# Kernel optimization log

Measured on AMD Instinct MI355X. Metric: run time of the kernel, lower is better.

Reference implementation:

```python
import jax, jax.numpy as jnp
import numpy as np

B, T, S, H = 8, 512, 512, 128


def setup_inputs() -> dict:
    key = jax.random.key(0)
    ks = jax.random.split(key, 8)
    query = jax.random.normal(ks[0], (B, T, H), dtype=jnp.float32)
    encoder_outputs = jax.random.normal(ks[1], (B, S, H), dtype=jnp.float32)
    src_lengths = jax.random.randint(ks[2], (B,), 1, S + 1)
    src_lengths = src_lengths.at[0].set(S)  # torch mask width == lengths.max() must equal S
    scale = 1.0 / np.sqrt(H)
    W_h = jax.random.normal(ks[3], (H, H), dtype=jnp.float32) * scale
    W_s = jax.random.normal(ks[4], (H, H), dtype=jnp.float32) * scale
    v = jax.random.normal(ks[5], (H,), dtype=jnp.float32) * scale
    W_out_w = jax.random.normal(ks[6], (H, 2 * H), dtype=jnp.float32) * (1.0 / np.sqrt(2 * H))
    W_out_b = jax.random.normal(ks[7], (H,), dtype=jnp.float32) * 0.01
    return {"query": query, "encoder_outputs": encoder_outputs,
            "src_lengths": src_lengths, "W_h": W_h, "W_s": W_s, "v": v,
            "W_out_w": W_out_w, "W_out_b": W_out_b}


def reference(query, encoder_outputs, src_lengths, W_h, W_s, v, W_out_w, W_out_b):
    # query: (B,T,H); encoder_outputs: (B,S,H)
    S_ = encoder_outputs.shape[1]
    WS = jnp.einsum('bth,oh->bto', query, W_s)            # (B,T,H)
    WH = jnp.einsum('bsh,oh->bso', encoder_outputs, W_h)  # (B,S,H)
    # additive scores: v^T tanh(W_s s_t + W_h h_i)  -> (B,T,S)
    scores = jnp.einsum('btsh,h->bts', jnp.tanh(WS[:, :, None, :] + WH[:, None, :, :]), v)
    mask = jnp.arange(S_) < src_lengths[:, None]          # (B,S)
    # faithful quirk: original zeroes (not -inf) masked scores before softmax
    scores = jnp.where(mask[:, None, :], scores, 0.0)
    attn = jax.nn.softmax(scores, axis=-1)                # (B,T,S)
    ct = jnp.einsum('bts,bsh->bth', attn, encoder_outputs)
    concat = jnp.concatenate([ct, query], axis=-1)        # (B,T,2H)
    return jnp.tanh(jnp.einsum('btc,oc->bto', concat, W_out_w) + W_out_b)
```

## Files before the change

### kernel.cpp

```cpp
#include <hip/hip_runtime.h>

#define NB 8
#define NT 512
#define NS 512
#define NH 128
#define C2LOG2E 2.8853900817779268f

__device__ __forceinline__ float fast_exp2(float x) { return __builtin_amdgcn_exp2f(x); }
__device__ __forceinline__ float fast_rcp(float x)  { return __builtin_amdgcn_rcpf(x); }
__device__ __forceinline__ float fast_tanh(float x) {
  float e = fast_exp2(x * C2LOG2E);
  return 1.0f - 2.0f * fast_rcp(e + 1.0f);
}

__device__ __forceinline__ float dot4(float4 a, float4 b) {
  return (a.x * b.x + a.y * b.y) + (a.z * b.z + a.w * b.w);
}

__device__ __forceinline__ float2 pair_acc2(float e0, float e1, float v0, float v1,
                                            float2 f0, float2 f1, float2 acc) {
  float2 P0, P1, num, den;
  P0.x = fmaf(e0, f0.x, 1.0f); P0.y = fmaf(e0, f0.y, 1.0f);
  P1.x = fmaf(e1, f1.x, 1.0f); P1.y = fmaf(e1, f1.y, 1.0f);
  num.x = fmaf(v0, P1.x, v1 * P0.x); num.y = fmaf(v0, P1.y, v1 * P0.y);
  den.x = P0.x * P1.x; den.y = P0.y * P1.y;
  acc.x = fmaf(num.x, fast_rcp(den.x), acc.x);
  acc.y = fmaf(num.y, fast_rcp(den.y), acc.y);
  return acc;
}

__global__ __launch_bounds__(256) void bah_proj_kernel(
    const float* __restrict__ query, const float* __restrict__ enc,
    const float* __restrict__ W_s, const float* __restrict__ W_h,
    const float* __restrict__ Wout, const float* __restrict__ Woutb,
    float* __restrict__ EWS, float* __restrict__ EWHT,
    float* __restrict__ ENCW, float* __restrict__ QW2) {
  __shared__ __align__(16) float lds_w[64 * 132];
  __shared__ __align__(16) float lds_x[32 * 132];
  const int set = blockIdx.x >> 8;
  const int blk = blockIdx.x & 255;
  const int rb = blk >> 1, ch = blk & 1;
  const int r0 = rb * 32, c0 = ch * 64;
  const int tid = threadIdx.x;
  const float* in = (set == 1 || set == 2) ? enc : query;
  const float* Wb; int wst;
  if (set == 0)      { Wb = W_s;        wst = 128; }
  else if (set == 1) { Wb = W_h;        wst = 128; }
  else if (set == 2) { Wb = Wout;       wst = 256; }
  else               { Wb = Wout + 128; wst = 256; }
  for (int i = tid; i < 2048; i += 256) {
    int r = i >> 5, c4 = i & 31;
    *(float4*)(lds_w + r * 132 + c4 * 4) =
        *(const float4*)(Wb + (c0 + r) * wst + c4 * 4);
  }
  for (int i = tid; i < 1024; i += 256) {
    int r = i >> 5, c4 = i & 31;
    *(float4*)(lds_x + r * 132 + c4 * 4) =
        *(const float4*)(in + (r0 + r) * NH + c4 * 4);
  }
  __syncthreads();
  const int cg = tid & 31;
  const int rg = tid >> 5;
  float acc[4][2] = {{0,0},{0,0},{0,0},{0,0}};
  for (int k4 = 0; k4 < 32; ++k4) {
    float4 xa[4], wb[2];
    #pragma unroll
    for (int i = 0; i < 4; ++i)
      xa[i] = *(const float4*)(lds_x + (rg * 4 + i) * 132 + k4 * 4);
    #pragma unroll
    for (int m = 0; m < 2; ++m)
      wb[m] = *(const float4*)(lds_w + (cg + 32 * m) * 132 + k4 * 4);
    #pragma unroll
    for (int i = 0; i < 4; ++i)
      #pragma unroll
      for (int m = 0; m < 2; ++m)
        acc[i][m] += dot4(xa[i], wb[m]);
  }
  if (set == 0) {
    #pragma unroll
    for (int i = 0; i < 4; ++i)
      #pragma unroll
      for (int m = 0; m < 2; ++m)
        EWS[(r0 + rg * 4 + i) * NH + c0 + cg + 32 * m] =
            fast_exp2(C2LOG2E * acc[i][m]);
  } else if (set == 1) {
    __syncthreads();
    #pragma unroll
    for (int i = 0; i < 4; ++i)
      #pragma unroll
      for (int m = 0; m < 2; ++m)
        lds_x[(cg + 32 * m) * 33 + rg * 4 + i] = fast_exp2(C2LOG2E * acc[i][m]);
    __syncthreads();
    const int b = r0 >> 9, sl0 = r0 & 511;
    const int s_lane = tid & 31, hr = tid >> 5;
    #pragma unroll
    for (int j = 0; j < 8; ++j)
      EWHT[b * NH * NS + (c0 + hr * 8 + j) * NS + sl0 + s_lane] =
          lds_x[(hr * 8 + j) * 33 + s_lane];
  } else if (set == 2) {
    #pragma unroll
    for (int i = 0; i < 4; ++i)
      #pragma unroll
      for (int m = 0; m < 2; ++m)
        ENCW[(r0 + rg * 4 + i) * NH + c0 + cg + 32 * m] = acc[i][m];
  } else {
    #pragma unroll
    for (int i = 0; i < 4; ++i)
      #pragma unroll
      for (int m = 0; m < 2; ++m) {
        int c = c0 + cg + 32 * m;
        QW2[(r0 + rg * 4 + i) * NH + c] = acc[i][m] + Woutb[c];
      }
  }
}

__global__ __launch_bounds__(512) void bah_mega_kernel(
    const float* __restrict__ EWS, const float* __restrict__ EWHT,
    const float* __restrict__ v, const float* __restrict__ ENCW,
    const float* __restrict__ QW2, const int* __restrict__ src_len,
    float* __restrict__ out) {
  __shared__ __align__(16) float smem[13824];
  float* s_v   = smem;
  float* s_et  = smem + 128;
  float* s_aT  = smem + 1184;
  float* s_par = smem + 5280;
  float* s_sc  = smem + 9632;
  float* s_red = smem + 13760;

  const int tid = threadIdx.x;
  const int bb = blockIdx.x >> 6;
  const int t0 = (blockIdx.x & 63) * 8;
  const int len = src_len[bb];

  if (tid < 32) *(float4*)(s_v + tid * 4) = *(const float4*)(v + tid * 4);
  if (tid < 256) {
    int r = tid >> 5, c4 = tid & 31;
    *(float4*)(s_et + r * 132 + c4 * 4) =
        *(const float4*)(EWS + (bb * NT + t0 + r) * NH + c4 * 4);
  }
  __syncthreads();

  float V0;
  {
    float2 vv = *(const float2*)(s_v + (tid & 63) * 2);
    V0 = vv.x + vv.y;
    #pragma unroll
    for (int msk = 1; msk <= 32; msk <<= 1)
      V0 += __shfl_xor(V0, msk, 64);
  }

  const int tg = tid >> 8, sp = tid & 255;
  const int sbase = sp * 2;
  const int h0 = tg * 64;
  float2 acc2[8];
  #pragma unroll
  for (int i = 0; i < 8; ++i) { acc2[i].x = 0.f; acc2[i].y = 0.f; }
  const int wave_s0 = (sp & ~63) * 2;
  if (wave_s0 < len) {
    const float* fb = EWHT + bb * NH * NS + h0 * NS + sbase;
    for (int ho = 0; ho < 8; ++ho) {
      const float* fh = fb + ho * 8 * NS;
      float2 F0 = *(const float2*)(fh + 0 * NS);
      float2 F1 = *(const float2*)(fh + 1 * NS);
      float2 F2 = *(const float2*)(fh + 2 * NS);
      float2 F3 = *(const float2*)(fh + 3 * NS);
      float2 F4 = *(const float2*)(fh + 4 * NS);
      float2 F5 = *(const float2*)(fh + 5 * NS);
      float2 F6 = *(const float2*)(fh + 6 * NS);
      float2 F7 = *(const float2*)(fh + 7 * NS);
      float4 va = *(const float4*)(s_v + h0 + ho * 8);
      float4 vb = *(const float4*)(s_v + h0 + ho * 8 + 4);
      #pragma unroll
      for (int tt = 0; tt < 8; ++tt) {
        float4 e0 = *(const float4*)(s_et + tt * 132 + h0 + ho * 8);
        float4 e1 = *(const float4*)(s_et + tt * 132 + h0 + ho * 8 + 4);
        acc2[tt] = pair_acc2(e0.x, e0.y, va.x, va.y, F0, F1, acc2[tt]);
        acc2[tt] = pair_acc2(e0.z, e0.w, va.z, va.w, F2, F3, acc2[tt]);
        acc2[tt] = pair_acc2(e1.x, e1.y, vb.x, vb.y, F4, F5, acc2[tt]);
        acc2[tt] = pair_acc2(e1.z, e1.w, vb.z, vb.w, F6, F7, acc2[tt]);
      }
    }
  }
  if (tg == 1) {
    #pragma unroll
    for (int tt = 0; tt < 8; ++tt)
      *(float2*)(s_par + sp * 17 + tt * 2) = acc2[tt];
  }
  __syncthreads();
  if (tg == 0) {
    #pragma unroll
    for (int tt = 0; tt < 8; ++tt) {
      float2 oth = *(const float2*)(s_par + sp * 17 + tt * 2);
      float sx = acc2[tt].x + oth.x;
      float sy = acc2[tt].y + oth.y;
      float2 r;
      r.x = (sbase + 0 < len) ? fmaf(-2.f, sx, V0) : 0.f;
      r.y = (sbase + 1 < len) ? fmaf(-2.f, sy, V0) : 0.f;
      *(float2*)(s_sc + tt * 516 + sbase) = r;
    }
  }
  __syncthreads();

  const int t = tid & 7;
  const int c = tid >> 3;
  const int wv = tid >> 6;
  float pv[8];
  float mx = -3.4e38f;
  #pragma unroll
  for (int k = 0; k < 8; ++k) {
    pv[k] = s_sc[t * 516 + c + 64 * k];
    mx = fmaxf(mx, pv[k]);
  }
  #pragma unroll
  for (int msk = 8; msk <= 32; msk <<= 1)
    mx = fmaxf(mx, __shfl_xor(mx, msk, 64));
  if ((tid & 63) < 8) s_red[wv * 8 + t] = mx;
  __syncthreads();
  #pragma unroll
  for (int j = 1; j < 8; ++j) mx = fmaxf(mx, s_red[j * 8 + t]);
  mx = fmaxf(mx, s_red[t]);
  __syncthreads();
  float sum = 0.f;
  #pragma unroll
  for (int k = 0; k < 8; ++k) {
    pv[k] = fast_exp2((pv[k] - mx) * 1.4426950408889634f);
    sum += pv[k];
  }
  #pragma unroll
  for (int msk = 8; msk <= 32; msk <<= 1)
    sum += __shfl_xor(sum, msk, 64);
  if ((tid & 63) < 8) s_red[wv * 8 + t] = sum;
  __syncthreads();
  sum = 0.f;
  #pragma unroll
  for (int j = 0; j < 8; ++j) sum += s_red[j * 8 + t];
  const float rd = fast_rcp(sum);
  #pragma unroll
  for (int k = 0; k < 8; ++k)
    s_aT[(c + 64 * k) * 8 + t] = pv[k] * rd;
  __syncthreads();

  const int hg = tid & 31, sg = tid >> 5;
  float4 a8[8] = {{0,0,0,0},{0,0,0,0},{0,0,0,0},{0,0,0,0},
                  {0,0,0,0},{0,0,0,0},{0,0,0,0},{0,0,0,0}};
  const float* eb = ENCW + bb * NS * NH + hg * 4;
  for (int k = 0; k < 32; ++k) {
    int s = sg * 32 + k;
    float4 e  = *(const float4*)(eb + s * NH);
    float4 w0 = *(const float4*)(s_aT + s * 8);
    float4 w1 = *(const float4*)(s_aT + s * 8 + 4);
    a8[0].x += w0.x*e.x; a8[0].y += w0.x*e.y; a8[0].z += w0.x*e.z; a8[0].w += w0.x*e.w;
    a8[1].x += w0.y*e.x; a8[1].y += w0.y*e.y; a8[1].z += w0.y*e.z; a8[1].w += w0.y*e.w;
    a8[2].x += w0.z*e.x; a8[2].y += w0.z*e.y; a8[2].z += w0.z*e.z; a8[2].w += w0.z*e.w;
    a8[3].x += w0.w*e.x; a8[3].y += w0.w*e.y; a8[3].z += w0.w*e.z; a8[3].w += w0.w*e.w;
    a8[4].x += w1.x*e.x; a8[4].y += w1.x*e.y; a8[4].z += w1.x*e.z; a8[4].w += w1.x*e.w;
    a8[5].x += w1.y*e.x; a8[5].y += w1.y*e.y; a8[5].z += w1.y*e.z; a8[5].w += w1.y*e.w;
    a8[6].x += w1.z*e.x; a8[6].y += w1.z*e.y; a8[6].z += w1.z*e.z; a8[6].w += w1.z*e.w;
    a8[7].x += w1.w*e.x; a8[7].y += w1.w*e.y; a8[7].z += w1.w*e.z; a8[7].w += w1.w*e.w;
  }
  #pragma unroll
  for (int i = 0; i < 8; ++i) {
    a8[i].x += __shfl_xor(a8[i].x, 32, 64);
    a8[i].y += __shfl_xor(a8[i].y, 32, 64);
    a8[i].z += __shfl_xor(a8[i].z, 32, 64);
    a8[i].w += __shfl_xor(a8[i].w, 32, 64);
  }
  float* lred = s_par;
  if ((tid & 63) < 32) {
    #pragma unroll
    for (int i = 0; i < 8; ++i)
      *(float4*)(lred + wv * 1024 + i * 128 + hg * 4) = a8[i];
  }
  __syncthreads();
  if (tid < 256) {
    int tt = tid >> 5, hh = tid & 31;
    float4 o = {0.f, 0.f, 0.f, 0.f};
    #pragma unroll
    for (int j = 0; j < 8; ++j) {
      float4 p = *(const float4*)(lred + j * 1024 + tt * 128 + hh * 4);
      o.x += p.x; o.y += p.y; o.z += p.z; o.w += p.w;
    }
    const int row = bb * NT + t0 + tt;
    float4 q4 = *(const float4*)(QW2 + row * NH + hh * 4);
    float4 r;
    r.x = fast_tanh(o.x + q4.x);
    r.y = fast_tanh(o.y + q4.y);
    r.z = fast_tanh(o.z + q4.z);
    r.w = fast_tanh(o.w + q4.w);
    *(float4*)(out + row * NH + hh * 4) = r;
  }
}

extern "C" void kernel_launch(void* const* d_in, const int* in_sizes, int n_in,
                              void* d_out, int out_size, void* d_ws, size_t ws_size,
                              hipStream_t stream) {
  const float* query = (const float*)d_in[0];
  const float* enc   = (const float*)d_in[1];
  const int*   slen  = (const int*)d_in[2];
  const float* W_h   = (const float*)d_in[3];
  const float* W_s   = (const float*)d_in[4];
  const float* v     = (const float*)d_in[5];
  const float* Woutw = (const float*)d_in[6];
  const float* Woutb = (const float*)d_in[7];
  float* out = (float*)d_out;

  float* ws = (float*)d_ws;
  float* EWS  = ws;
  float* EWHT = ws + 524288;
  float* ENCW = ws + 1048576;
  float* QW2  = ws + 1572864;

  bah_proj_kernel<<<1024, 256, 0, stream>>>(query, enc, W_s, W_h, Woutw,
                                            Woutb, EWS, EWHT, ENCW, QW2);
  bah_mega_kernel<<<512, 512, 0, stream>>>(EWS, EWHT, v, ENCW, QW2, slen, out);
}
```

Baseline: 118.1 us.

## Retile attention kernel to 4 queries per block with 4 keys per thread

The fused attention kernel now handles 4 query rows per block with 256 threads instead of 8 rows with 512, and each thread covers 4 source positions using float4 loads of the transposed encoder projection. Shared memory shrinks through buffer aliasing, and launch bounds ask for 4 blocks per CU so more blocks can be resident. The grid doubles to 1024 blocks. In exchange, each EWHT element loaded is reused across only 4 query rows instead of 8, so global and L2 traffic for the score stage roughly doubles.

```diff
diff --git a/kernel.cpp b/kernel.cpp
--- a/kernel.cpp
+++ b/kernel.cpp
@@ -17,15 +17,21 @@
   return (a.x * b.x + a.y * b.y) + (a.z * b.z + a.w * b.w);
 }
 
-__device__ __forceinline__ float2 pair_acc2(float e0, float e1, float v0, float v1,
-                                            float2 f0, float2 f1, float2 acc) {
-  float2 P0, P1, num, den;
+__device__ __forceinline__ float4 pair_acc(float e0, float e1, float v0, float v1,
+                                           float4 f0, float4 f1, float4 acc) {
+  float4 P0, P1, num, den;
   P0.x = fmaf(e0, f0.x, 1.0f); P0.y = fmaf(e0, f0.y, 1.0f);
+  P0.z = fmaf(e0, f0.z, 1.0f); P0.w = fmaf(e0, f0.w, 1.0f);
   P1.x = fmaf(e1, f1.x, 1.0f); P1.y = fmaf(e1, f1.y, 1.0f);
+  P1.z = fmaf(e1, f1.z, 1.0f); P1.w = fmaf(e1, f1.w, 1.0f);
   num.x = fmaf(v0, P1.x, v1 * P0.x); num.y = fmaf(v0, P1.y, v1 * P0.y);
+  num.z = fmaf(v0, P1.z, v1 * P0.z); num.w = fmaf(v0, P1.w, v1 * P0.w);
   den.x = P0.x * P1.x; den.y = P0.y * P1.y;
+  den.z = P0.z * P1.z; den.w = P0.w * P1.w;
   acc.x = fmaf(num.x, fast_rcp(den.x), acc.x);
   acc.y = fmaf(num.y, fast_rcp(den.y), acc.y);
+  acc.z = fmaf(num.z, fast_rcp(den.z), acc.z);
+  acc.w = fmaf(num.w, fast_rcp(den.w), acc.w);
   return acc;
 }
 
@@ -114,26 +120,27 @@
   }
 }
 
-__global__ __launch_bounds__(512) void bah_mega_kernel(
+__global__ __launch_bounds__(256, 4) void bah_mega_kernel(
     const float* __restrict__ EWS, const float* __restrict__ EWHT,
     const float* __restrict__ v, const float* __restrict__ ENCW,
     const float* __restrict__ QW2, const int* __restrict__ src_len,
     float* __restrict__ out) {
-  __shared__ __align__(16) float smem[13824];
-  float* s_v   = smem;
-  float* s_et  = smem + 128;
-  float* s_aT  = smem + 1184;
-  float* s_par = smem + 5280;
-  float* s_sc  = smem + 9632;
-  float* s_red = smem + 13760;
+  __shared__ __align__(16) float smem[4928];
+  float* s_aT  = smem;
+  float* s_par = smem;
+  float* s_sc  = smem + 2176;
+  float* lred  = smem + 2176;
+  float* s_et  = smem + 4240;
+  float* s_v   = smem + 4768;
+  float* s_red = smem + 4896;
 
   const int tid = threadIdx.x;
-  const int bb = blockIdx.x >> 6;
-  const int t0 = (blockIdx.x & 63) * 8;
+  const int bb = blockIdx.x >> 7;
+  const int t0 = (blockIdx.x & 127) * 4;
   const int len = src_len[bb];
 
   if (tid < 32) *(float4*)(s_v + tid * 4) = *(const float4*)(v + tid * 4);
-  if (tid < 256) {
+  if (tid < 128) {
     int r = tid >> 5, c4 = tid & 31;
     *(float4*)(s_et + r * 132 + c4 * 4) =
         *(const float4*)(EWS + (bb * NT + t0 + r) * NH + c4 * 4);
@@ -149,60 +156,58 @@
       V0 += __shfl_xor(V0, msk, 64);
   }
 
-  const int tg = tid >> 8, sp = tid & 255;
-  const int sbase = sp * 2;
+  const int tg = tid >> 7, sp = tid & 127;
+  const int sbase = sp * 4;
   const int h0 = tg * 64;
-  float2 acc2[8];
-  #pragma unroll
-  for (int i = 0; i < 8; ++i) { acc2[i].x = 0.f; acc2[i].y = 0.f; }
-  const int wave_s0 = (sp & ~63) * 2;
+  float4 acc4[4] = {{0,0,0,0},{0,0,0,0},{0,0,0,0},{0,0,0,0}};
+  const int wave_s0 = (sp & 64) * 4;
   if (wave_s0 < len) {
     const float* fb = EWHT + bb * NH * NS + h0 * NS + sbase;
     for (int ho = 0; ho < 8; ++ho) {
       const float* fh = fb + ho * 8 * NS;
-      float2 F0 = *(const float2*)(fh + 0 * NS);
-      float2 F1 = *(const float2*)(fh + 1 * NS);
-      float2 F2 = *(const float2*)(fh + 2 * NS);
-      float2 F3 = *(const float2*)(fh + 3 * NS);
-      float2 F4 = *(const float2*)(fh + 4 * NS);
-      float2 F5 = *(const float2*)(fh + 5 * NS);
-      float2 F6 = *(const float2*)(fh + 6 * NS);
-      float2 F7 = *(const float2*)(fh + 7 * NS);
+      float4 F0 = *(const float4*)(fh + 0 * NS);
+      float4 F1 = *(const float4*)(fh + 1 * NS);
+      float4 F2 = *(const float4*)(fh + 2 * NS);
+      float4 F3 = *(const float4*)(fh + 3 * NS);
+      float4 F4 = *(const float4*)(fh + 4 * NS);
+      float4 F5 = *(const float4*)(fh + 5 * NS);
+      float4 F6 = *(const float4*)(fh + 6 * NS);
+      float4 F7 = *(const float4*)(fh + 7 * NS);
       float4 va = *(const float4*)(s_v + h0 + ho * 8);
       float4 vb = *(const float4*)(s_v + h0 + ho * 8 + 4);
       #pragma unroll
-      for (int tt = 0; tt < 8; ++tt) {
+      for (int tt = 0; tt < 4; ++tt) {
         float4 e0 = *(const float4*)(s_et + tt * 132 + h0 + ho * 8);
         float4 e1 = *(const float4*)(s_et + tt * 132 + h0 + ho * 8 + 4);
-        acc2[tt] = pair_acc2(e0.x, e0.y, va.x, va.y, F0, F1, acc2[tt]);
-        acc2[tt] = pair_acc2(e0.z, e0.w, va.z, va.w, F2, F3, acc2[tt]);
-        acc2[tt] = pair_acc2(e1.x, e1.y, vb.x, vb.y, F4, F5, acc2[tt]);
-        acc2[tt] = pair_acc2(e1.z, e1.w, vb.z, vb.w, F6, F7, acc2[tt]);
+        acc4[tt] = pair_acc(e0.x, e0.y, va.x, va.y, F0, F1, acc4[tt]);
+        acc4[tt] = pair_acc(e0.z, e0.w, va.z, va.w, F2, F3, acc4[tt]);
+        acc4[tt] = pair_acc(e1.x, e1.y, vb.x, vb.y, F4, F5, acc4[tt]);
+        acc4[tt] = pair_acc(e1.z, e1.w, vb.z, vb.w, F6, F7, acc4[tt]);
       }
     }
   }
   if (tg == 1) {
     #pragma unroll
-    for (int tt = 0; tt < 8; ++tt)
-      *(float2*)(s_par + sp * 17 + tt * 2) = acc2[tt];
+    for (int tt = 0; tt < 4; ++tt)
+      *(float4*)(s_par + sp * 17 + tt * 4) = acc4[tt];
   }
   __syncthreads();
   if (tg == 0) {
     #pragma unroll
-    for (int tt = 0; tt < 8; ++tt) {
-      float2 oth = *(const float2*)(s_par + sp * 17 + tt * 2);
-      float sx = acc2[tt].x + oth.x;
-      float sy = acc2[tt].y + oth.y;
-      float2 r;
-      r.x = (sbase + 0 < len) ? fmaf(-2.f, sx, V0) : 0.f;
-      r.y = (sbase + 1 < len) ? fmaf(-2.f, sy, V0) : 0.f;
-      *(float2*)(s_sc + tt * 516 + sbase) = r;
+    for (int tt = 0; tt < 4; ++tt) {
+      float4 oth = *(const float4*)(s_par + sp * 17 + tt * 4);
+      float4 r;
+      r.x = (sbase + 0 < len) ? fmaf(-2.f, acc4[tt].x + oth.x, V0) : 0.f;
+      r.y = (sbase + 1 < len) ? fmaf(-2.f, acc4[tt].y + oth.y, V0) : 0.f;
+      r.z = (sbase + 2 < len) ? fmaf(-2.f, acc4[tt].z + oth.z, V0) : 0.f;
+      r.w = (sbase + 3 < len) ? fmaf(-2.f, acc4[tt].w + oth.w, V0) : 0.f;
+      *(float4*)(s_sc + tt * 516 + sbase) = r;
     }
   }
   __syncthreads();
 
-  const int t = tid & 7;
-  const int c = tid >> 3;
+  const int t = tid & 3;
+  const int c = tid >> 2;
   const int wv = tid >> 6;
   float pv[8];
   float mx = -3.4e38f;
@@ -212,13 +217,12 @@
     mx = fmaxf(mx, pv[k]);
   }
   #pragma unroll
-  for (int msk = 8; msk <= 32; msk <<= 1)
+  for (int msk = 4; msk <= 32; msk <<= 1)
     mx = fmaxf(mx, __shfl_xor(mx, msk, 64));
-  if ((tid & 63) < 8) s_red[wv * 8 + t] = mx;
-  __syncthreads();
-  #pragma unroll
-  for (int j = 1; j < 8; ++j) mx = fmaxf(mx, s_red[j * 8 + t]);
-  mx = fmaxf(mx, s_red[t]);
+  if ((tid & 63) < 4) s_red[wv * 4 + t] = mx;
+  __syncthreads();
+  mx = fmaxf(fmaxf(s_red[t], s_red[4 + t]),
+             fmaxf(s_red[8 + t], s_red[12 + t]));
   __syncthreads();
   float sum = 0.f;
   #pragma unroll
@@ -227,66 +231,55 @@
     sum += pv[k];
   }
   #pragma unroll
-  for (int msk = 8; msk <= 32; msk <<= 1)
+  for (int msk = 4; msk <= 32; msk <<= 1)
     sum += __shfl_xor(sum, msk, 64);
-  if ((tid & 63) < 8) s_red[wv * 8 + t] = sum;
-  __syncthreads();
-  sum = 0.f;
-  #pragma unroll
-  for (int j = 0; j < 8; ++j) sum += s_red[j * 8 + t];
+  if ((tid & 63) < 4) s_red[wv * 4 + t] = sum;
+  __syncthreads();
+  sum = (s_red[t] + s_red[4 + t]) + (s_red[8 + t] + s_red[12 + t]);
   const float rd = fast_rcp(sum);
   #pragma unroll
   for (int k = 0; k < 8; ++k)
-    s_aT[(c + 64 * k) * 8 + t] = pv[k] * rd;
+    s_aT[(c + 64 * k) * 4 + t] = pv[k] * rd;
   __syncthreads();
 
   const int hg = tid & 31, sg = tid >> 5;
-  float4 a8[8] = {{0,0,0,0},{0,0,0,0},{0,0,0,0},{0,0,0,0},
-                  {0,0,0,0},{0,0,0,0},{0,0,0,0},{0,0,0,0}};
+  float4 a4[4] = {{0,0,0,0},{0,0,0,0},{0,0,0,0},{0,0,0,0}};
   const float* eb = ENCW + bb * NS * NH + hg * 4;
-  for (int k = 0; k < 32; ++k) {
-    int s = sg * 32 + k;
-    float4 e  = *(const float4*)(eb + s * NH);
-    float4 w0 = *(const float4*)(s_aT + s * 8);
-    float4 w1 = *(const float4*)(s_aT + s * 8 + 4);
-    a8[0].x += w0.x*e.x; a8[0].y += w0.x*e.y; a8[0].z += w0.x*e.z; a8[0].w += w0.x*e.w;
-    a8[1].x += w0.y*e.x; a8[1].y += w0.y*e.y; a8[1].z += w0.y*e.z; a8[1].w += w0.y*e.w;
-    a8[2].x += w0.z*e.x; a8[2].y += w0.z*e.y; a8[2].z += w0.z*e.z; a8[2].w += w0.z*e.w;
-    a8[3].x += w0.w*e.x; a8[3].y += w0.w*e.y; a8[3].z += w0.w*e.z; a8[3].w += w0.w*e.w;
-    a8[4].x += w1.x*e.x; a8[4].y += w1.x*e.y; a8[4].z += w1.x*e.z; a8[4].w += w1.x*e.w;
-    a8[5].x += w1.y*e.x; a8[5].y += w1.y*e.y; a8[5].z += w1.y*e.z; a8[5].w += w1.y*e.w;
-    a8[6].x += w1.z*e.x; a8[6].y += w1.z*e.y; a8[6].z += w1.z*e.z; a8[6].w += w1.z*e.w;
-    a8[7].x += w1.w*e.x; a8[7].y += w1.w*e.y; a8[7].z += w1.w*e.z; a8[7].w += w1.w*e.w;
-  }
-  #pragma unroll
-  for (int i = 0; i < 8; ++i) {
-    a8[i].x += __shfl_xor(a8[i].x, 32, 64);
-    a8[i].y += __shfl_xor(a8[i].y, 32, 64);
-    a8[i].z += __shfl_xor(a8[i].z, 32, 64);
-    a8[i].w += __shfl_xor(a8[i].w, 32, 64);
-  }
-  float* lred = s_par;
+  for (int k = 0; k < 64; ++k) {
+    int s = sg * 64 + k;
+    float4 e = *(const float4*)(eb + s * NH);
+    float4 w = *(const float4*)(s_aT + s * 4);
+    a4[0].x += w.x*e.x; a4[0].y += w.x*e.y; a4[0].z += w.x*e.z; a4[0].w += w.x*e.w;
+    a4[1].x += w.y*e.x; a4[1].y += w.y*e.y; a4[1].z += w.y*e.z; a4[1].w += w.y*e.w;
+    a4[2].x += w.z*e.x; a4[2].y += w.z*e.y; a4[2].z += w.z*e.z; a4[2].w += w.z*e.w;
+    a4[3].x += w.w*e.x; a4[3].y += w.w*e.y; a4[3].z += w.w*e.z; a4[3].w += w.w*e.w;
+  }
+  #pragma unroll
+  for (int i = 0; i < 4; ++i) {
+    a4[i].x += __shfl_xor(a4[i].x, 32, 64);
+    a4[i].y += __shfl_xor(a4[i].y, 32, 64);
+    a4[i].z += __shfl_xor(a4[i].z, 32, 64);
+    a4[i].w += __shfl_xor(a4[i].w, 32, 64);
+  }
   if ((tid & 63) < 32) {
     #pragma unroll
-    for (int i = 0; i < 8; ++i)
-      *(float4*)(lred + wv * 1024 + i * 128 + hg * 4) = a8[i];
-  }
-  __syncthreads();
-  if (tid < 256) {
+    for (int i = 0; i < 4; ++i)
+      *(float4*)(lred + wv * 512 + i * 128 + hg * 4) = a4[i];
+  }
+  __syncthreads();
+  if (tid < 128) {
     int tt = tid >> 5, hh = tid & 31;
-    float4 o = {0.f, 0.f, 0.f, 0.f};
-    #pragma unroll
-    for (int j = 0; j < 8; ++j) {
-      float4 p = *(const float4*)(lred + j * 1024 + tt * 128 + hh * 4);
-      o.x += p.x; o.y += p.y; o.z += p.z; o.w += p.w;
-    }
+    float4 s0 = *(const float4*)(lred + 0 * 512 + tt * 128 + hh * 4);
+    float4 s1 = *(const float4*)(lred + 1 * 512 + tt * 128 + hh * 4);
+    float4 s2 = *(const float4*)(lred + 2 * 512 + tt * 128 + hh * 4);
+    float4 s3 = *(const float4*)(lred + 3 * 512 + tt * 128 + hh * 4);
     const int row = bb * NT + t0 + tt;
     float4 q4 = *(const float4*)(QW2 + row * NH + hh * 4);
     float4 r;
-    r.x = fast_tanh(o.x + q4.x);
-    r.y = fast_tanh(o.y + q4.y);
-    r.z = fast_tanh(o.z + q4.z);
-    r.w = fast_tanh(o.w + q4.w);
+    r.x = fast_tanh(((s0.x + s1.x) + (s2.x + s3.x)) + q4.x);
+    r.y = fast_tanh(((s0.y + s1.y) + (s2.y + s3.y)) + q4.y);
+    r.z = fast_tanh(((s0.z + s1.z) + (s2.z + s3.z)) + q4.z);
+    r.w = fast_tanh(((s0.w + s1.w) + (s2.w + s3.w)) + q4.w);
     *(float4*)(out + row * NH + hh * 4) = r;
   }
 }
@@ -312,5 +305,5 @@
 
   bah_proj_kernel<<<1024, 256, 0, stream>>>(query, enc, W_s, W_h, Woutw,
                                             Woutb, EWS, EWHT, ENCW, QW2);
-  bah_mega_kernel<<<512, 512, 0, stream>>>(EWS, EWHT, v, ENCW, QW2, slen, out);
-}
+  bah_mega_kernel<<<1024, 256, 0, stream>>>(EWS, EWHT, v, ENCW, QW2, slen, out);
+}
```

Result: slower. 129.8 us (+10.0%).

## Shrink shared memory via aliasing and tree reduction, interleave batch across blocks

Applied to the files above, without the earlier changes.

Cuts the kernel's shared-memory footprint by aliasing buffers whose lifetimes do not overlap and by replacing the 8-way partial-sum buffer with a three-step tree reduction. It also sets a min-blocks hint in launch_bounds and maps consecutive blocks to different batches. The goal is more resident blocks per CU and better load balance across the variable-length batches. In exchange, the final reduction adds several extra barriers and ends with only one wave computing the output.

```diff
diff --git a/kernel.cpp b/kernel.cpp
--- a/kernel.cpp
+++ b/kernel.cpp
@@ -114,22 +114,23 @@
   }
 }
 
-__global__ __launch_bounds__(512) void bah_mega_kernel(
+__global__ __launch_bounds__(512, 8) void bah_mega_kernel(
     const float* __restrict__ EWS, const float* __restrict__ EWHT,
     const float* __restrict__ v, const float* __restrict__ ENCW,
     const float* __restrict__ QW2, const int* __restrict__ src_len,
     float* __restrict__ out) {
-  __shared__ __align__(16) float smem[13824];
-  float* s_v   = smem;
-  float* s_et  = smem + 128;
-  float* s_aT  = smem + 1184;
-  float* s_par = smem + 5280;
-  float* s_sc  = smem + 9632;
-  float* s_red = smem + 13760;
+  __shared__ __align__(16) float smem[9472];
+  float* s_par = smem;
+  float* s_aT  = smem;
+  float* s_sc  = smem + 4096;
+  float* red4  = smem + 4096;
+  float* s_et  = smem + 8224;
+  float* s_v   = smem + 9280;
+  float* s_red = smem + 9408;
 
   const int tid = threadIdx.x;
-  const int bb = blockIdx.x >> 6;
-  const int t0 = (blockIdx.x & 63) * 8;
+  const int bb = blockIdx.x & 7;
+  const int t0 = (blockIdx.x >> 3) * 8;
   const int len = src_len[bb];
 
   if (tid < 32) *(float4*)(s_v + tid * 4) = *(const float4*)(v + tid * 4);
@@ -184,13 +185,13 @@
   if (tg == 1) {
     #pragma unroll
     for (int tt = 0; tt < 8; ++tt)
-      *(float2*)(s_par + sp * 17 + tt * 2) = acc2[tt];
+      *(float2*)(s_par + tt * 512 + sp * 2) = acc2[tt];
   }
   __syncthreads();
   if (tg == 0) {
     #pragma unroll
     for (int tt = 0; tt < 8; ++tt) {
-      float2 oth = *(const float2*)(s_par + sp * 17 + tt * 2);
+      float2 oth = *(const float2*)(s_par + tt * 512 + sp * 2);
       float sx = acc2[tt].x + oth.x;
       float sy = acc2[tt].y + oth.y;
       float2 r;
@@ -265,29 +266,55 @@
     a8[i].z += __shfl_xor(a8[i].z, 32, 64);
     a8[i].w += __shfl_xor(a8[i].w, 32, 64);
   }
-  float* lred = s_par;
-  if ((tid & 63) < 32) {
+  const int lane = tid & 63;
+  const bool lo = lane < 32;
+  if (wv >= 4 && lo) {
     #pragma unroll
     for (int i = 0; i < 8; ++i)
-      *(float4*)(lred + wv * 1024 + i * 128 + hg * 4) = a8[i];
-  }
-  __syncthreads();
-  if (tid < 256) {
-    int tt = tid >> 5, hh = tid & 31;
-    float4 o = {0.f, 0.f, 0.f, 0.f};
-    #pragma unroll
-    for (int j = 0; j < 8; ++j) {
-      float4 p = *(const float4*)(lred + j * 1024 + tt * 128 + hh * 4);
-      o.x += p.x; o.y += p.y; o.z += p.z; o.w += p.w;
-    }
-    const int row = bb * NT + t0 + tt;
-    float4 q4 = *(const float4*)(QW2 + row * NH + hh * 4);
-    float4 r;
-    r.x = fast_tanh(o.x + q4.x);
-    r.y = fast_tanh(o.y + q4.y);
-    r.z = fast_tanh(o.z + q4.z);
-    r.w = fast_tanh(o.w + q4.w);
-    *(float4*)(out + row * NH + hh * 4) = r;
+      *(float4*)(red4 + (wv - 4) * 1024 + i * 128 + hg * 4) = a8[i];
+  }
+  __syncthreads();
+  if (wv < 4 && lo) {
+    #pragma unroll
+    for (int i = 0; i < 8; ++i) {
+      float4 p = *(const float4*)(red4 + wv * 1024 + i * 128 + hg * 4);
+      a8[i].x += p.x; a8[i].y += p.y; a8[i].z += p.z; a8[i].w += p.w;
+    }
+  }
+  __syncthreads();
+  if (wv >= 2 && wv < 4 && lo) {
+    #pragma unroll
+    for (int i = 0; i < 8; ++i)
+      *(float4*)(red4 + (wv - 2) * 1024 + i * 128 + hg * 4) = a8[i];
+  }
+  __syncthreads();
+  if (wv < 2 && lo) {
+    #pragma unroll
+    for (int i = 0; i < 8; ++i) {
+      float4 p = *(const float4*)(red4 + wv * 1024 + i * 128 + hg * 4);
+      a8[i].x += p.x; a8[i].y += p.y; a8[i].z += p.z; a8[i].w += p.w;
+    }
+  }
+  __syncthreads();
+  if (wv == 1 && lo) {
+    #pragma unroll
+    for (int i = 0; i < 8; ++i)
+      *(float4*)(red4 + i * 128 + hg * 4) = a8[i];
+  }
+  __syncthreads();
+  if (wv == 0 && lo) {
+    #pragma unroll
+    for (int i = 0; i < 8; ++i) {
+      float4 p = *(const float4*)(red4 + i * 128 + hg * 4);
+      const int row = bb * NT + t0 + i;
+      float4 q4 = *(const float4*)(QW2 + row * NH + hg * 4);
+      float4 r;
+      r.x = fast_tanh(a8[i].x + p.x + q4.x);
+      r.y = fast_tanh(a8[i].y + p.y + q4.y);
+      r.z = fast_tanh(a8[i].z + p.z + q4.z);
+      r.w = fast_tanh(a8[i].w + p.w + q4.w);
+      *(float4*)(out + row * NH + hg * 4) = r;
+    }
   }
 }
 
```

After: 126.5 us. 7.2% more time.
